# Kernel optimization log

Measured on AMD Instinct MI355X. Metric: run time of the kernel, lower is better.

## Reference

```python
import jax, jax.numpy as jnp
import numpy as np

B, S, H = 16, 2048, 1024

def setup_inputs() -> dict:
    key = jax.random.key(0)
    k1, k2, k3, k4 = jax.random.split(key, 4)
    x = jax.random.normal(k1, (B, S, H), dtype=jnp.float32)
    # nn.Linear weights, stored as (out, in); y = x @ W.T
    scale = 1.0 / np.sqrt(H)
    W_q = jax.random.uniform(k2, (H, H), jnp.float32, -scale, scale)
    W_k = jax.random.uniform(k3, (H, H), jnp.float32, -scale, scale)
    W_v = jax.random.uniform(k4, (H, H), jnp.float32, -scale, scale)
    return {"x": x, "W_q": W_q, "W_k": W_k, "W_v": W_v}

def reference(x, W_q, W_k, W_v):
    # x: (B,S,H); W_*: (H,H) torch Linear layout (out,in)
    Q = jnp.einsum('bsh,oh->bso', x, W_q)
    K = jnp.einsum('bsh,oh->bso', x, W_k)
    V = jnp.einsum('bsh,oh->bso', x, W_v)
    scale = jnp.asarray(x.shape[-1] ** 0.5, dtype=x.dtype)
    energy = jnp.einsum('bqd,bkd->bqk', Q, K) / scale      # (B,S,S)
    attn = jax.nn.softmax(energy, axis=-1)                  # (B,S,S)
    attended = jnp.einsum('bqk,bkd->bqd', attn, V)          # (B,S,H)
    context = attended.mean(axis=1)                         # (B,H)
    attn_weights = attn.mean(axis=1)                        # (B,S)
    return (context, attn_weights)
```

## Files before the change

kernel.cpp:

```cpp
#include <hip/hip_runtime.h>
#include <hip/hip_bf16.h>
#include <stdint.h>

#define BB 16
#define SS 2048
#define HH 1024

using bf16 = __hip_bfloat16;
typedef __attribute__((ext_vector_type(8))) short short8;
typedef __attribute__((ext_vector_type(4))) float f32x4;

typedef unsigned int __attribute__((address_space(1))) as1_uint;
typedef unsigned int __attribute__((address_space(3))) as3_uint;

static constexpr size_t WS_XB   = 0;
static constexpr size_t WS_G    = 67108864;
static constexpr size_t WS_P    = 134217728;
static constexpr size_t WS_WQT  = 134217728;
static constexpr size_t WS_WKT  = 136314880;
static constexpr size_t WS_MT   = 138412032;
static constexpr size_t WS_LSUM = 201326592;
static constexpr size_t WS_T    = 201457664;
static constexpr size_t WS_NEED = 201523200;

__device__ __forceinline__ void async_copy16(bf16* lds_dst, const bf16* gsrc) {
    __builtin_amdgcn_global_load_lds((const as1_uint*)gsrc, (as3_uint*)lds_dst, 16, 0, 0);
}

__device__ __forceinline__ float bf2f(unsigned short u) {
    union { unsigned i; float f; } v; v.i = (unsigned)u << 16; return v.f;
}

__device__ __forceinline__ unsigned char f32_to_e4m3(float x) {
#if __has_builtin(__builtin_amdgcn_cvt_pk_fp8_f32)
    return (unsigned char)(__builtin_amdgcn_cvt_pk_fp8_f32(x, x, 0, false) & 0xff);
#else
    if (x >= 0.015625f) {
        union { float f; unsigned u; } v; v.f = x;
        int e = (v.u >> 23) & 0xff;
        unsigned m = v.u & 0x7fffff;
        unsigned mant = m >> 20;
        unsigned rem = m & 0xfffff;
        mant += (rem > 0x80000u) || (rem == 0x80000u && (mant & 1));
        int oe = e - 120;
        if (mant == 8) { mant = 0; oe += 1; }
        return (unsigned char)((oe << 3) | mant);
    }
    int code = (int)rintf(x * 512.0f);
    return (unsigned char)code;
#endif
}

__device__ __forceinline__ float e4m3_to_f32(unsigned char b) {
#if __has_builtin(__builtin_amdgcn_cvt_pk_f32_fp8)
    auto v = __builtin_amdgcn_cvt_pk_f32_fp8((int)b, false);
    return v[0];
#else
    int e = (b >> 3) & 15, m = b & 7;
    if (e) { union { unsigned u; float f; } v; v.u = ((unsigned)(e + 120) << 23) | ((unsigned)m << 20); return v.f; }
    return (float)m * 0.001953125f;
#endif
}

__global__ __launch_bounds__(256) void cast_x_kernel(const float* __restrict__ x,
                                                     bf16* __restrict__ xb, int n4) {
    int stride = gridDim.x * blockDim.x;
    for (int i = blockIdx.x * blockDim.x + threadIdx.x; i < n4; i += stride) {
        float4 v = reinterpret_cast<const float4*>(x)[i];
        union { bf16 h[4]; uint2 u; } p;
        p.h[0] = __float2bfloat16(v.x); p.h[1] = __float2bfloat16(v.y);
        p.h[2] = __float2bfloat16(v.z); p.h[3] = __float2bfloat16(v.w);
        reinterpret_cast<uint2*>(xb)[i] = p.u;
    }
}

__global__ __launch_bounds__(256) void transpose_w_kernel(const float* __restrict__ wq,
                                                          const float* __restrict__ wk,
                                                          bf16* __restrict__ wqT,
                                                          bf16* __restrict__ wkT) {
    __shared__ float tile[64][65];
    const float* src = blockIdx.z ? wk : wq;
    bf16* dst = blockIdx.z ? wkT : wqT;
    const int o0 = blockIdx.y * 64, i0 = blockIdx.x * 64;
    const int tr = threadIdx.x >> 4;
    const int tc = (threadIdx.x & 15) * 4;
#pragma unroll
    for (int k = 0; k < 4; ++k) {
        float4 v = *reinterpret_cast<const float4*>(src + (size_t)(o0 + tr + k * 16) * 1024 + i0 + tc);
        tile[tr + k * 16][tc + 0] = v.x; tile[tr + k * 16][tc + 1] = v.y;
        tile[tr + k * 16][tc + 2] = v.z; tile[tr + k * 16][tc + 3] = v.w;
    }
    __syncthreads();
#pragma unroll
    for (int k = 0; k < 4; ++k) {
        int ri = tr + k * 16;
        union { bf16 h[4]; uint2 u; } p;
#pragma unroll
        for (int j = 0; j < 4; ++j) p.h[j] = __float2bfloat16(tile[tc + j][ri]);
        *reinterpret_cast<uint2*>(dst + (size_t)(i0 + ri) * 1024 + o0 + tc) = p.u;
    }
}

__global__ __launch_bounds__(256) void gemm_mt64(const bf16* __restrict__ wkT,
                                                 const bf16* __restrict__ wqT,
                                                 bf16* __restrict__ Mt) {
    __shared__ bf16 As[64 * 64], Bs[64 * 64];
    f32x4 acc[2][2];
#pragma unroll
    for (int m = 0; m < 2; ++m)
#pragma unroll
        for (int n = 0; n < 2; ++n) { acc[m][n][0]=0.f; acc[m][n][1]=0.f; acc[m][n][2]=0.f; acc[m][n][3]=0.f; }
    const int tid = threadIdx.x, wid = tid >> 6, lane = tid & 63;
    const int wm = wid >> 1, wn = wid & 1;
    const int srow = lane >> 3, scol = (lane & 7) * 8;
    const bf16* Ab = wkT + (size_t)blockIdx.y * 64 * 1024;
    const bf16* Bb = wqT + (size_t)blockIdx.x * 64 * 1024;
    for (int kt = 0; kt < 1024; kt += 64) {
#pragma unroll
        for (int i = 0; i < 2; ++i) {
            int row0 = i * 32 + wid * 8;
            async_copy16(As + row0 * 64, Ab + (size_t)(row0 + srow) * 1024 + kt + scol);
            async_copy16(Bs + row0 * 64, Bb + (size_t)(row0 + srow) * 1024 + kt + scol);
        }
        __syncthreads();
#pragma unroll
        for (int kk = 0; kk < 2; ++kk) {
            short8 a[2], b[2];
#pragma unroll
            for (int m = 0; m < 2; ++m)
                a[m] = *reinterpret_cast<const short8*>(
                    As + (wm * 32 + m * 16 + (lane & 15)) * 64 + kk * 32 + (lane >> 4) * 8);
#pragma unroll
            for (int n = 0; n < 2; ++n)
                b[n] = *reinterpret_cast<const short8*>(
                    Bs + (wn * 32 + n * 16 + (lane & 15)) * 64 + kk * 32 + (lane >> 4) * 8);
#pragma unroll
            for (int m = 0; m < 2; ++m)
#pragma unroll
                for (int n = 0; n < 2; ++n)
                    acc[m][n] = __builtin_amdgcn_mfma_f32_16x16x32_bf16(a[m], b[n], acc[m][n], 0, 0, 0);
        }
        __syncthreads();
    }
    const int row0 = blockIdx.y * 64 + wm * 32 + ((lane >> 4) << 2);
    const int col0 = blockIdx.x * 64 + wn * 32 + (lane & 15);
#pragma unroll
    for (int m = 0; m < 2; ++m)
#pragma unroll
        for (int n = 0; n < 2; ++n)
#pragma unroll
            for (int r = 0; r < 4; ++r)
                Mt[(size_t)(row0 + m * 16 + r) * 1024 + col0 + n * 16] =
                    __float2bfloat16(acc[m][n][r] * 0.03125f);
}

static constexpr int NT256 = 16;

__device__ __forceinline__ void stage_A256(char* As_base, int qm,
                                           const bf16* __restrict__ Ag, int kt) {
    const int tid = threadIdx.x;
    const int wid = tid >> 6;
#pragma unroll
    for (int i = 0; i < 2; ++i) {
        int beta = (i * 512 + tid) * 16;
        int rho  = beta >> 7;
        int c    = beta & 127;
        int cs   = c ^ ((rho & 7) << 4);
        int wm_r = rho >> 6, j = rho & 63;
        int grow = wm_r * 128 + qm * 64 + j;
        const bf16* src = Ag + (size_t)grow * 1024 + kt * 64 + (cs >> 1);
        char* dst = As_base + qm * 16384 + i * 8192 + wid * 1024;
        async_copy16((bf16*)dst, src);
    }
}

__device__ __forceinline__ void stage_B256(char* Bs_base, int qn,
                                           const bf16* __restrict__ Bg, int kt) {
    const int tid = threadIdx.x;
    const int wid = tid >> 6;
#pragma unroll
    for (int i = 0; i < 2; ++i) {
        int beta = (i * 512 + tid) * 16;
        int rho  = beta >> 7;
        int c    = beta & 127;
        int cs   = c ^ ((rho & 7) << 4);
        int wn_r = rho >> 5, s = rho & 31;
        int grow = wn_r * 64 + qn * 32 + s;
        const bf16* src = Bg + (size_t)grow * 1024 + kt * 64 + (cs >> 1);
        char* dst = Bs_base + qn * 16384 + i * 8192 + wid * 1024;
        async_copy16((bf16*)dst, src);
    }
}

__device__ __forceinline__ void gemm256_mainloop(const bf16* __restrict__ Ag,
                                                 const bf16* __restrict__ Bg,
                                                 char* lds, f32x4 acc[8][4]) {
    const int tid = threadIdx.x;
    const int lane = tid & 63;
    const int wm = (tid >> 6) >> 2;
    const int wn = (tid >> 6) & 3;

#pragma unroll
    for (int m = 0; m < 8; ++m)
#pragma unroll
        for (int n = 0; n < 4; ++n) { acc[m][n][0]=0.f; acc[m][n][1]=0.f; acc[m][n][2]=0.f; acc[m][n][3]=0.f; }

    char* A0 = lds;            char* B0 = lds + 32768;
    char* A1 = lds + 65536;    char* B1 = lds + 98304;

    stage_A256(A0, 0, Ag, 0);
    stage_B256(B0, 0, Bg, 0);
    stage_B256(B0, 1, Bg, 0);
    stage_A256(A0, 1, Ag, 0);
    stage_A256(A1, 0, Ag, 1);
    stage_B256(B1, 0, Bg, 1);
    asm volatile("s_waitcnt vmcnt(4)" ::: "memory");
    __builtin_amdgcn_s_barrier();

    short8 a[4][2], b0[2][2], b1[2][2];

#pragma unroll 1
    for (int t = 0; t < NT256; ++t) {
        char* As  = (t & 1) ? A1 : A0;
        char* Bs  = (t & 1) ? B1 : B0;
        char* Aso = (t & 1) ? A0 : A1;
        char* Bso = (t & 1) ? B0 : B1;

#pragma unroll
        for (int mi = 0; mi < 4; ++mi)
#pragma unroll
            for (int kk = 0; kk < 2; ++kk) {
                int row = wm * 64 + mi * 16 + (lane & 15);
                int off = (row * 128 + kk * 64 + (lane >> 4) * 16) ^ ((row & 7) << 4);
                a[mi][kk] = *reinterpret_cast<const short8*>(As + off);
            }
#pragma unroll
        for (int ni = 0; ni < 2; ++ni)
#pragma unroll
            for (int kk = 0; kk < 2; ++kk) {
                int row = wn * 32 + ni * 16 + (lane & 15);
                int off = (row * 128 + kk * 64 + (lane >> 4) * 16) ^ ((row & 7) << 4);
                b0[ni][kk] = *reinterpret_cast<const short8*>(Bs + off);
            }
        if (t + 1 < NT256) stage_B256(Bso, 1, Bg, t + 1);
        __builtin_amdgcn_s_barrier();
        asm volatile("s_waitcnt lgkmcnt(0)" ::: "memory");
        __builtin_amdgcn_s_setprio(1);
#pragma unroll
        for (int mi = 0; mi < 4; ++mi)
#pragma unroll
            for (int ni = 0; ni < 2; ++ni)
#pragma unroll
                for (int kk = 0; kk < 2; ++kk)
                    acc[mi][ni] = __builtin_amdgcn_mfma_f32_16x16x32_bf16(
                        a[mi][kk], b0[ni][kk], acc[mi][ni], 0, 0, 0);
        __builtin_amdgcn_s_setprio(0);
        __builtin_amdgcn_s_barrier();

#pragma unroll
        for (int ni = 0; ni < 2; ++ni)
#pragma unroll
            for (int kk = 0; kk < 2; ++kk) {
                int row = 128 + wn * 32 + ni * 16 + (lane & 15);
                int off = (row * 128 + kk * 64 + (lane >> 4) * 16) ^ ((row & 7) << 4);
                b1[ni][kk] = *reinterpret_cast<const short8*>(Bs + off);
            }
        if (t + 1 < NT256) stage_A256(Aso, 1, Ag, t + 1);
        __builtin_amdgcn_s_barrier();
        asm volatile("s_waitcnt lgkmcnt(0)" ::: "memory");
        __builtin_amdgcn_s_setprio(1);
#pragma unroll
        for (int mi = 0; mi < 4; ++mi)
#pragma unroll
            for (int ni = 0; ni < 2; ++ni)
#pragma unroll
                for (int kk = 0; kk < 2; ++kk)
                    acc[mi][2 + ni] = __builtin_amdgcn_mfma_f32_16x16x32_bf16(
                        a[mi][kk], b1[ni][kk], acc[mi][2 + ni], 0, 0, 0);
        __builtin_amdgcn_s_setprio(0);
        __builtin_amdgcn_s_barrier();

#pragma unroll
        for (int mi = 0; mi < 4; ++mi)
#pragma unroll
            for (int kk = 0; kk < 2; ++kk) {
                int row = 128 + wm * 64 + mi * 16 + (lane & 15);
                int off = (row * 128 + kk * 64 + (lane >> 4) * 16) ^ ((row & 7) << 4);
                a[mi][kk] = *reinterpret_cast<const short8*>(As + off);
            }
        if (t + 2 < NT256) stage_A256(As, 0, Ag, t + 2);
        __builtin_amdgcn_s_barrier();
        asm volatile("s_waitcnt lgkmcnt(0)" ::: "memory");
        __builtin_amdgcn_s_setprio(1);
#pragma unroll
        for (int mi = 0; mi < 4; ++mi)
#pragma unroll
            for (int ni = 0; ni < 2; ++ni)
#pragma unroll
                for (int kk = 0; kk < 2; ++kk)
                    acc[4 + mi][2 + ni] = __builtin_amdgcn_mfma_f32_16x16x32_bf16(
                        a[mi][kk], b1[ni][kk], acc[4 + mi][2 + ni], 0, 0, 0);
        __builtin_amdgcn_s_setprio(0);
        __builtin_amdgcn_s_barrier();

        if (t + 2 < NT256) stage_B256(Bs, 0, Bg, t + 2);
        __builtin_amdgcn_s_barrier();
        __builtin_amdgcn_s_setprio(1);
#pragma unroll
        for (int mi = 0; mi < 4; ++mi)
#pragma unroll
            for (int ni = 0; ni < 2; ++ni)
#pragma unroll
                for (int kk = 0; kk < 2; ++kk)
                    acc[4 + mi][ni] = __builtin_amdgcn_mfma_f32_16x16x32_bf16(
                        a[mi][kk], b0[ni][kk], acc[4 + mi][ni], 0, 0, 0);
        __builtin_amdgcn_s_setprio(0);
        if (t + 2 < NT256) asm volatile("s_waitcnt vmcnt(4)" ::: "memory");
        else               asm volatile("s_waitcnt vmcnt(0)" ::: "memory");
        __builtin_amdgcn_s_barrier();
    }
}

__global__ __launch_bounds__(512, 2) void gemm_g256(const bf16* __restrict__ xb,
                                                    const bf16* __restrict__ Mt,
                                                    bf16* __restrict__ G) {
    extern __shared__ char lds[];
    f32x4 acc[8][4];
    const int bx = blockIdx.x, by = blockIdx.y;
    gemm256_mainloop(xb + (size_t)by * 256 * 1024, Mt + (size_t)bx * 256 * 1024, lds, acc);
    const int lane = threadIdx.x & 63, wid = threadIdx.x >> 6;
    const int wm = wid >> 2, wn = wid & 3;
    const int row0 = by * 256 + wm * 128 + ((lane >> 4) << 2);
    const int col0 = bx * 256 + wn * 64 + (lane & 15);
#pragma unroll
    for (int mi = 0; mi < 8; ++mi)
#pragma unroll
        for (int ni = 0; ni < 4; ++ni)
#pragma unroll
            for (int r = 0; r < 4; ++r)
                G[(size_t)(row0 + mi * 16 + r) * 1024 + col0 + ni * 16] =
                    __float2bfloat16(acc[mi][ni][r]);
}

__global__ __launch_bounds__(512, 2) void energy_fused256(const bf16* __restrict__ G,
                                                          const bf16* __restrict__ xb,
                                                          unsigned char* __restrict__ P,
                                                          float* __restrict__ lsum) {
    extern __shared__ char lds[];
    f32x4 acc[8][4];
    const int bx = blockIdx.x, by = blockIdx.y, bz = blockIdx.z;
    gemm256_mainloop(G + (size_t)(bz * 2048 + by * 256) * 1024,
                     xb + (size_t)(bz * 2048 + bx * 256) * 1024, lds, acc);
    const int lane = threadIdx.x & 63, wid = threadIdx.x >> 6;
    const int wm = wid >> 2, wn = wid & 3;
    const int q0 = bz * 2048 + by * 256 + wm * 128 + ((lane >> 4) << 2);
    const int k0 = bx * 256 + wn * 64 + (lane & 15);
#pragma unroll
    for (int mi = 0; mi < 8; ++mi) {
        float s[4] = {0.f, 0.f, 0.f, 0.f};
#pragma unroll
        for (int ni = 0; ni < 4; ++ni)
#pragma unroll
            for (int r = 0; r < 4; ++r) {
                float e = __expf(acc[mi][ni][r]);
                unsigned char c = f32_to_e4m3(e);
                P[(size_t)(q0 + mi * 16 + r) * 2048 + k0 + ni * 16] = c;
                s[r] += e4m3_to_f32(c);
            }
#pragma unroll
        for (int off = 1; off < 16; off <<= 1)
#pragma unroll
            for (int r = 0; r < 4; ++r) s[r] += __shfl_xor(s[r], off, 64);
        if ((lane & 15) == 0) {
#pragma unroll
            for (int r = 0; r < 4; ++r) atomicAdd(&lsum[q0 + mi * 16 + r], s[r]);
        }
    }
}

__global__ __launch_bounds__(256) void colsum_kernel(const unsigned char* __restrict__ P,
                                                     const float* __restrict__ lsum,
                                                     float* __restrict__ aw) {
    const int b = blockIdx.y, qc = blockIdx.x, t = threadIdx.x;
    float acc[8] = {0.f, 0.f, 0.f, 0.f, 0.f, 0.f, 0.f, 0.f};
    const unsigned char* base = P + (size_t)(b * 2048 + qc * 128) * 2048 + t * 8;
    const float* ls = lsum + b * 2048 + qc * 128;
    for (int q = 0; q < 128; ++q) {
        float w = 1.0f / ls[q];
        uint2 v = *reinterpret_cast<const uint2*>(base + (size_t)q * 2048);
#if __has_builtin(__builtin_amdgcn_cvt_pk_f32_fp8)
        auto p0 = __builtin_amdgcn_cvt_pk_f32_fp8((int)v.x, false);
        auto p1 = __builtin_amdgcn_cvt_pk_f32_fp8((int)v.x, true);
        auto p2 = __builtin_amdgcn_cvt_pk_f32_fp8((int)v.y, false);
        auto p3 = __builtin_amdgcn_cvt_pk_f32_fp8((int)v.y, true);
        acc[0] += p0[0] * w; acc[1] += p0[1] * w;
        acc[2] += p1[0] * w; acc[3] += p1[1] * w;
        acc[4] += p2[0] * w; acc[5] += p2[1] * w;
        acc[6] += p3[0] * w; acc[7] += p3[1] * w;
#else
        unsigned char by8[8];
        *reinterpret_cast<uint2*>(by8) = v;
#pragma unroll
        for (int j = 0; j < 8; ++j) acc[j] += e4m3_to_f32(by8[j]) * w;
#endif
    }
#pragma unroll
    for (int j = 0; j < 8; ++j)
        atomicAdd(&aw[b * 2048 + t * 8 + j], acc[j] * (1.0f / 2048.0f));
}

__global__ __launch_bounds__(256) void av_x_kernel(const float* __restrict__ aw,
                                                   const bf16* __restrict__ xb,
                                                   float* __restrict__ t) {
    const int b = blockIdx.y;
    const int kc = blockIdx.x;
    const int tid = threadIdx.x;
    float4 acc = {0.f, 0.f, 0.f, 0.f};
    const int k0 = kc * 128;
#pragma unroll 4
    for (int k = k0; k < k0 + 128; ++k) {
        float w = aw[b * 2048 + k];
        uint2 v = *reinterpret_cast<const uint2*>(xb + (size_t)(b * 2048 + k) * 1024 + tid * 4);
        acc.x += w * bf2f((unsigned short)(v.x & 0xffff));
        acc.y += w * bf2f((unsigned short)(v.x >> 16));
        acc.z += w * bf2f((unsigned short)(v.y & 0xffff));
        acc.w += w * bf2f((unsigned short)(v.y >> 16));
    }
    float* tp = t + b * 1024 + tid * 4;
    atomicAdd(tp + 0, acc.x); atomicAdd(tp + 1, acc.y);
    atomicAdd(tp + 2, acc.z); atomicAdd(tp + 3, acc.w);
}

__global__ __launch_bounds__(256) void ctx_gemv_kernel(const float* __restrict__ t,
                                                       const float* __restrict__ wv,
                                                       float* __restrict__ ctx) {
    const int b = blockIdx.y;
    const int wid = threadIdx.x >> 6, lane = threadIdx.x & 63;
    const int o = blockIdx.x * 4 + wid;
    const float4* t4 = reinterpret_cast<const float4*>(t + b * 1024);
    const float4* w4 = reinterpret_cast<const float4*>(wv + (size_t)o * 1024);
    float s = 0.f;
#pragma unroll
    for (int j = lane; j < 256; j += 64) {
        float4 a = t4[j], w = w4[j];
        s += a.x * w.x + a.y * w.y + a.z * w.z + a.w * w.w;
    }
#pragma unroll
    for (int off = 1; off < 64; off <<= 1) s += __shfl_xor(s, off, 64);
    if (lane == 0) ctx[b * 1024 + o] = s;
}

__global__ void ws_too_small_kernel(float* out) {
    if (threadIdx.x == 0 && blockIdx.x == 0) out[0] = 12345.0f;
}

extern "C" void kernel_launch(void* const* d_in, const int* in_sizes, int n_in,
                              void* d_out, int out_size, void* d_ws, size_t ws_size,
                              hipStream_t stream) {
    const float* x  = (const float*)d_in[0];
    const float* wq = (const float*)d_in[1];
    const float* wk = (const float*)d_in[2];
    const float* wv = (const float*)d_in[3];
    float* out = (float*)d_out;
    float* ctx = out;
    float* aw  = out + 16384;

    if (ws_size < WS_NEED) {
        hipMemsetAsync(d_out, 0, (size_t)out_size * sizeof(float), stream);
        ws_too_small_kernel<<<1, 64, 0, stream>>>(out);
        return;
    }

    char* ws = (char*)d_ws;
    bf16* xb   = (bf16*)(ws + WS_XB);
    bf16* G    = (bf16*)(ws + WS_G);
    unsigned char* P = (unsigned char*)(ws + WS_P);
    bf16* wqT  = (bf16*)(ws + WS_WQT);
    bf16* wkT  = (bf16*)(ws + WS_WKT);
    bf16* Mt   = (bf16*)(ws + WS_MT);
    float* lsum = (float*)(ws + WS_LSUM);
    float* t    = (float*)(ws + WS_T);

    hipMemsetAsync(d_out, 0, (size_t)out_size * sizeof(float), stream);
    hipMemsetAsync(lsum, 0, 131072 + 65536, stream);

    cast_x_kernel<<<2048, 256, 0, stream>>>(x, xb, (BB * SS * HH) / 4);
    transpose_w_kernel<<<dim3(16, 16, 2), 256, 0, stream>>>(wq, wk, wqT, wkT);

    gemm_mt64<<<dim3(16, 16), 256, 0, stream>>>(wkT, wqT, Mt);
    gemm_g256<<<dim3(4, 128), 512, 131072, stream>>>(xb, Mt, G);

    energy_fused256<<<dim3(8, 8, 16), 512, 131072, stream>>>(G, xb, P, lsum);
    colsum_kernel<<<dim3(16, 16), 256, 0, stream>>>(P, lsum, aw);

    av_x_kernel<<<dim3(16, 16), 256, 0, stream>>>(aw, xb, t);
    ctx_gemv_kernel<<<dim3(256, 16), 256, 0, stream>>>(t, wv, ctx);
}
```

Before: 324.4 us.

## Merge GEMM main-loop phases into two barrier stages with precomputed offsets

Restructures the 256x256 bf16 GEMM main loop from four barrier-separated phases into two. Each phase now loads a larger set of A/B fragments from LDS and issues A and B async global-to-LDS staging together. Global source offsets and LDS read offsets are precomputed once outside the loop, so per-iteration address arithmetic drops out. The aim is fewer barriers and less scalar/vector address work. In exchange, more fragment registers (b0 and b1) are live at once, and the ordering of prefetch writes relative to buffer reads changes, which could cause hazards.

```diff
diff --git a/kernel.cpp b/kernel.cpp
--- a/kernel.cpp
+++ b/kernel.cpp
@@ -156,49 +156,14 @@
 
 static constexpr int NT256 = 16;
 
-__device__ __forceinline__ void stage_A256(char* As_base, int qm,
-                                           const bf16* __restrict__ Ag, int kt) {
-    const int tid = threadIdx.x;
-    const int wid = tid >> 6;
-#pragma unroll
-    for (int i = 0; i < 2; ++i) {
-        int beta = (i * 512 + tid) * 16;
-        int rho  = beta >> 7;
-        int c    = beta & 127;
-        int cs   = c ^ ((rho & 7) << 4);
-        int wm_r = rho >> 6, j = rho & 63;
-        int grow = wm_r * 128 + qm * 64 + j;
-        const bf16* src = Ag + (size_t)grow * 1024 + kt * 64 + (cs >> 1);
-        char* dst = As_base + qm * 16384 + i * 8192 + wid * 1024;
-        async_copy16((bf16*)dst, src);
-    }
-}
-
-__device__ __forceinline__ void stage_B256(char* Bs_base, int qn,
-                                           const bf16* __restrict__ Bg, int kt) {
-    const int tid = threadIdx.x;
-    const int wid = tid >> 6;
-#pragma unroll
-    for (int i = 0; i < 2; ++i) {
-        int beta = (i * 512 + tid) * 16;
-        int rho  = beta >> 7;
-        int c    = beta & 127;
-        int cs   = c ^ ((rho & 7) << 4);
-        int wn_r = rho >> 5, s = rho & 31;
-        int grow = wn_r * 64 + qn * 32 + s;
-        const bf16* src = Bg + (size_t)grow * 1024 + kt * 64 + (cs >> 1);
-        char* dst = Bs_base + qn * 16384 + i * 8192 + wid * 1024;
-        async_copy16((bf16*)dst, src);
-    }
-}
-
 __device__ __forceinline__ void gemm256_mainloop(const bf16* __restrict__ Ag,
                                                  const bf16* __restrict__ Bg,
                                                  char* lds, f32x4 acc[8][4]) {
     const int tid = threadIdx.x;
     const int lane = tid & 63;
-    const int wm = (tid >> 6) >> 2;
-    const int wn = (tid >> 6) & 3;
+    const int wid = tid >> 6;
+    const int wm = wid >> 2;
+    const int wn = wid & 3;
 
 #pragma unroll
     for (int m = 0; m < 8; ++m)
@@ -208,12 +173,53 @@
     char* A0 = lds;            char* B0 = lds + 32768;
     char* A1 = lds + 65536;    char* B1 = lds + 98304;
 
-    stage_A256(A0, 0, Ag, 0);
-    stage_B256(B0, 0, Bg, 0);
-    stage_B256(B0, 1, Bg, 0);
-    stage_A256(A0, 1, Ag, 0);
-    stage_A256(A1, 0, Ag, 1);
-    stage_B256(B1, 0, Bg, 1);
+    int soA[2], soB[2];
+    {
+#pragma unroll
+        for (int i = 0; i < 2; ++i) {
+            int beta = (i * 512 + tid) * 16;
+            int rho  = beta >> 7;
+            int cs   = (beta & 127) ^ ((rho & 7) << 4);
+            soA[i] = ((rho >> 6) * 128 + (rho & 63)) * 1024 + (cs >> 1);
+            soB[i] = ((rho >> 5) * 64  + (rho & 31)) * 1024 + (cs >> 1);
+        }
+    }
+    const int dstw = wid * 1024;
+
+    int roA[4], roB[2];
+    {
+        const int swz = (lane & 7) << 4;
+        const int colb = (lane >> 4) * 16;
+#pragma unroll
+        for (int mi = 0; mi < 4; ++mi) {
+            int row = wm * 64 + mi * 16 + (lane & 15);
+            roA[mi] = (row * 128 + colb) ^ swz;
+        }
+#pragma unroll
+        for (int ni = 0; ni < 2; ++ni) {
+            int row = wn * 32 + ni * 16 + (lane & 15);
+            roB[ni] = (row * 128 + colb) ^ swz;
+        }
+    }
+
+#define STAGE_A256(buf, q, kt)                                                        \
+    {                                                                                 \
+        async_copy16((bf16*)((buf) + (q) * 16384 + dstw),                             \
+                     Ag + soA[0] + (q) * 65536 + (kt) * 64);                          \
+        async_copy16((bf16*)((buf) + (q) * 16384 + 8192 + dstw),                      \
+                     Ag + soA[1] + (q) * 65536 + (kt) * 64);                          \
+    }
+#define STAGE_B256(buf, q, kt)                                                        \
+    {                                                                                 \
+        async_copy16((bf16*)((buf) + (q) * 16384 + dstw),                             \
+                     Bg + soB[0] + (q) * 32768 + (kt) * 64);                          \
+        async_copy16((bf16*)((buf) + (q) * 16384 + 8192 + dstw),                      \
+                     Bg + soB[1] + (q) * 32768 + (kt) * 64);                          \
+    }
+
+    STAGE_A256(A0, 0, 0); STAGE_A256(A0, 1, 0);
+    STAGE_B256(B0, 0, 0); STAGE_B256(B0, 1, 0);
+    STAGE_A256(A1, 0, 1); STAGE_B256(B1, 0, 1);
     asm volatile("s_waitcnt vmcnt(4)" ::: "memory");
     __builtin_amdgcn_s_barrier();
 
@@ -227,22 +233,18 @@
         char* Bso = (t & 1) ? B0 : B1;
 
 #pragma unroll
-        for (int mi = 0; mi < 4; ++mi)
-#pragma unroll
-            for (int kk = 0; kk < 2; ++kk) {
-                int row = wm * 64 + mi * 16 + (lane & 15);
-                int off = (row * 128 + kk * 64 + (lane >> 4) * 16) ^ ((row & 7) << 4);
-                a[mi][kk] = *reinterpret_cast<const short8*>(As + off);
-            }
-#pragma unroll
-        for (int ni = 0; ni < 2; ++ni)
-#pragma unroll
-            for (int kk = 0; kk < 2; ++kk) {
-                int row = wn * 32 + ni * 16 + (lane & 15);
-                int off = (row * 128 + kk * 64 + (lane >> 4) * 16) ^ ((row & 7) << 4);
-                b0[ni][kk] = *reinterpret_cast<const short8*>(Bs + off);
-            }
-        if (t + 1 < NT256) stage_B256(Bso, 1, Bg, t + 1);
+        for (int mi = 0; mi < 4; ++mi) {
+            a[mi][0] = *reinterpret_cast<const short8*>(As + roA[mi]);
+            a[mi][1] = *reinterpret_cast<const short8*>(As + (roA[mi] ^ 64));
+        }
+#pragma unroll
+        for (int ni = 0; ni < 2; ++ni) {
+            b0[ni][0] = *reinterpret_cast<const short8*>(Bs + roB[ni]);
+            b0[ni][1] = *reinterpret_cast<const short8*>(Bs + (roB[ni] ^ 64));
+            b1[ni][0] = *reinterpret_cast<const short8*>(Bs + (roB[ni] + 16384));
+            b1[ni][1] = *reinterpret_cast<const short8*>(Bs + ((roB[ni] ^ 64) + 16384));
+        }
+        if (t + 1 < NT256) { STAGE_A256(Aso, 1, t + 1); STAGE_B256(Bso, 1, t + 1); }
         __builtin_amdgcn_s_barrier();
         asm volatile("s_waitcnt lgkmcnt(0)" ::: "memory");
         __builtin_amdgcn_s_setprio(1);
@@ -254,21 +256,6 @@
                 for (int kk = 0; kk < 2; ++kk)
                     acc[mi][ni] = __builtin_amdgcn_mfma_f32_16x16x32_bf16(
                         a[mi][kk], b0[ni][kk], acc[mi][ni], 0, 0, 0);
-        __builtin_amdgcn_s_setprio(0);
-        __builtin_amdgcn_s_barrier();
-
-#pragma unroll
-        for (int ni = 0; ni < 2; ++ni)
-#pragma unroll
-            for (int kk = 0; kk < 2; ++kk) {
-                int row = 128 + wn * 32 + ni * 16 + (lane & 15);
-                int off = (row * 128 + kk * 64 + (lane >> 4) * 16) ^ ((row & 7) << 4);
-                b1[ni][kk] = *reinterpret_cast<const short8*>(Bs + off);
-            }
-        if (t + 1 < NT256) stage_A256(Aso, 1, Ag, t + 1);
-        __builtin_amdgcn_s_barrier();
-        asm volatile("s_waitcnt lgkmcnt(0)" ::: "memory");
-        __builtin_amdgcn_s_setprio(1);
 #pragma unroll
         for (int mi = 0; mi < 4; ++mi)
 #pragma unroll
@@ -281,14 +268,11 @@
         __builtin_amdgcn_s_barrier();
 
 #pragma unroll
-        for (int mi = 0; mi < 4; ++mi)
-#pragma unroll
-            for (int kk = 0; kk < 2; ++kk) {
-                int row = 128 + wm * 64 + mi * 16 + (lane & 15);
-                int off = (row * 128 + kk * 64 + (lane >> 4) * 16) ^ ((row & 7) << 4);
-                a[mi][kk] = *reinterpret_cast<const short8*>(As + off);
-            }
-        if (t + 2 < NT256) stage_A256(As, 0, Ag, t + 2);
+        for (int mi = 0; mi < 4; ++mi) {
+            a[mi][0] = *reinterpret_cast<const short8*>(As + (roA[mi] + 16384));
+            a[mi][1] = *reinterpret_cast<const short8*>(As + ((roA[mi] ^ 64) + 16384));
+        }
+        if (t + 2 < NT256) { STAGE_A256(As, 0, t + 2); STAGE_B256(Bs, 0, t + 2); }
         __builtin_amdgcn_s_barrier();
         asm volatile("s_waitcnt lgkmcnt(0)" ::: "memory");
         __builtin_amdgcn_s_setprio(1);
@@ -300,12 +284,6 @@
                 for (int kk = 0; kk < 2; ++kk)
                     acc[4 + mi][2 + ni] = __builtin_amdgcn_mfma_f32_16x16x32_bf16(
                         a[mi][kk], b1[ni][kk], acc[4 + mi][2 + ni], 0, 0, 0);
-        __builtin_amdgcn_s_setprio(0);
-        __builtin_amdgcn_s_barrier();
-
-        if (t + 2 < NT256) stage_B256(Bs, 0, Bg, t + 2);
-        __builtin_amdgcn_s_barrier();
-        __builtin_amdgcn_s_setprio(1);
 #pragma unroll
         for (int mi = 0; mi < 4; ++mi)
 #pragma unroll
@@ -319,6 +297,8 @@
         else               asm volatile("s_waitcnt vmcnt(0)" ::: "memory");
         __builtin_amdgcn_s_barrier();
     }
+#undef STAGE_A256
+#undef STAGE_B256
 }
 
 __global__ __launch_bounds__(512, 2) void gemm_g256(const bf16* __restrict__ xb,
```

After: 322.9 us. About the same (-0.4%).
